# Kernel tuning notes

Hardware: AMD Instinct MI355X
Metric: run time of the kernel (lower is better)

## Reference

```python
import jax, jax.numpy as jnp
import numpy as np

HEADS = 8
DIM_HEAD = 64
DIM_COOR = 3
SCALE = (DIM_COOR * DIM_HEAD) ** -0.5


def setup_inputs() -> dict:
    key = jax.random.key(0)
    k1, k2, k3 = jax.random.split(key, 3)
    x = jax.random.normal(k1, (2, 2048, 256, 3), dtype=jnp.float32)
    w_qkv = jax.random.normal(k2, (1536, 256), dtype=jnp.float32)
    w_out = jax.random.normal(k3, (256, 512), dtype=jnp.float32)
    return {"x": x, "w_qkv": w_qkv, "w_out": w_out}


def reference(x, w_qkv, w_out):
    b, n, _, c = x.shape
    # VNLinear: contract feature dim, keep coord dim  -> [b, n, 3*h*d, c]
    qkv = jnp.einsum('bnic,oi->bnoc', x, w_qkv)
    q, k, v = jnp.split(qkv, 3, axis=-2)  # each [b, n, h*d, c]

    def to_heads(t):
        return t.reshape(b, n, HEADS, DIM_HEAD, c).transpose(0, 2, 1, 3, 4)  # b h n d c

    q, k, v = map(to_heads, (q, k, v))
    q = q * SCALE
    # scores sum over head-dim AND coordinate-dim
    sim = jnp.einsum('bhidc,bhjdc->bhij', q, k)
    attn = jax.nn.softmax(sim, axis=-1)
    out = jnp.einsum('bhij,bhjdc->bhidc', attn, v)  # coord dim preserved
    out = out.transpose(0, 2, 1, 3, 4).reshape(b, n, HEADS * DIM_HEAD, c)
    return jnp.einsum('bnic,oi->bnoc', out, w_out)
```

## Files before the change

### kernel.cpp

```cpp
#include <hip/hip_runtime.h>
#include <hip/hip_bf16.h>

#define SCALE 0.07216878364870322f

typedef __bf16 bf16x8 __attribute__((ext_vector_type(8)));
typedef float f32x16 __attribute__((ext_vector_type(16)));
typedef float f32x4v __attribute__((ext_vector_type(4)));
typedef unsigned int u32x4 __attribute__((ext_vector_type(4)));
typedef unsigned short u16;

#define MFMA(a, b, c) __builtin_amdgcn_mfma_f32_32x32x16_bf16(a, b, c, 0, 0, 0)

__device__ __forceinline__ u16 b16(float v) { return __builtin_bit_cast(u16, (__bf16)v); }
__device__ __forceinline__ float fb16(u16 u) {
    unsigned int t = (unsigned int)u << 16;
    return __builtin_bit_cast(float, t);
}
__device__ __forceinline__ unsigned int splitpack(float v) {
    u16 h = b16(v);
    float r = v - fb16(h);
    return (unsigned int)h | ((unsigned int)b16(r) << 16);
}
__device__ __forceinline__ unsigned int pack2(float a, float b) {
    return (unsigned int)b16(a) | ((unsigned int)b16(b) << 16);
}

__global__ __launch_bounds__(256) void qkv_mfma(const float* __restrict__ x,
                                                const float* __restrict__ wq,
                                                u16* __restrict__ Qhi, u16* __restrict__ Qlo,
                                                u16* __restrict__ Khi, u16* __restrict__ Klo,
                                                u16* __restrict__ Vf) {
    __shared__ unsigned int ldsr[2][32][196];
    const int tid = threadIdx.x;
    const int lane = tid & 63, w = tid >> 6, hf = lane >> 5, l31 = lane & 31;
    const int o0 = blockIdx.x * 64;
    const int n0 = blockIdx.y * 128;
    const int b = blockIdx.z;
    const int nw0 = n0 + w * 32;
    const int part = o0 >> 9;
    const int h = (o0 >> 6) & 7;
    const int bh = b * 8 + h;

    const float* xp = x + ((size_t)(b * 2048 + nw0 + l31)) * 768 + hf * 24;
    const float* wp0 = wq + (size_t)(o0 + l31) * 256 + hf * 8;
    const float* wp1 = wp0 + 32 * 256;

    f32x16 acc[3][2] = {};
    #pragma unroll 2
    for (int k0 = 0; k0 < 16; ++k0) {
        float xf[24], wf0[8], wf1[8];
        #pragma unroll
        for (int q = 0; q < 6; ++q) {
            f32x4v t = *(const f32x4v*)(xp + k0 * 48 + q * 4);
            xf[q * 4 + 0] = t[0]; xf[q * 4 + 1] = t[1];
            xf[q * 4 + 2] = t[2]; xf[q * 4 + 3] = t[3];
        }
        {
            f32x4v t0 = *(const f32x4v*)(wp0 + k0 * 16);
            f32x4v t1 = *(const f32x4v*)(wp0 + k0 * 16 + 4);
            f32x4v t2 = *(const f32x4v*)(wp1 + k0 * 16);
            f32x4v t3 = *(const f32x4v*)(wp1 + k0 * 16 + 4);
            #pragma unroll
            for (int e = 0; e < 4; ++e) {
                wf0[e] = t0[e]; wf0[4 + e] = t1[e];
                wf1[e] = t2[e]; wf1[4 + e] = t3[e];
            }
        }
        bf16x8 xh[3], xl[3], wh[2], wl[2];
        #pragma unroll
        for (int c = 0; c < 3; ++c)
            #pragma unroll
            for (int e = 0; e < 8; ++e) {
                float v = xf[e * 3 + c];
                __bf16 hi = (__bf16)v;
                xh[c][e] = hi;
                xl[c][e] = (__bf16)(v - (float)hi);
            }
        #pragma unroll
        for (int e = 0; e < 8; ++e) {
            { float v = wf0[e]; __bf16 hi = (__bf16)v; wh[0][e] = hi; wl[0][e] = (__bf16)(v - (float)hi); }
            { float v = wf1[e]; __bf16 hi = (__bf16)v; wh[1][e] = hi; wl[1][e] = (__bf16)(v - (float)hi); }
        }
        #pragma unroll
        for (int c = 0; c < 3; ++c)
            #pragma unroll
            for (int ot = 0; ot < 2; ++ot) {
                acc[c][ot] = MFMA(xh[c], wh[ot], acc[c][ot]);
                acc[c][ot] = MFMA(xl[c], wh[ot], acc[c][ot]);
                acc[c][ot] = MFMA(xh[c], wl[ot], acc[c][ot]);
            }
    }

    #pragma unroll
    for (int round = 0; round < 2; ++round) {
        __syncthreads();
        if ((w >> 1) == round) {
            unsigned int (*L)[196] = ldsr[w & 1];
            #pragma unroll
            for (int c = 0; c < 3; ++c)
                #pragma unroll
                for (int ot = 0; ot < 2; ++ot)
                    #pragma unroll
                    for (int r = 0; r < 16; ++r) {
                        float v = acc[c][ot][r];
                        if (part == 0) v *= SCALE;
                        int nn = (r & 3) + 8 * (r >> 2) + 4 * hf;
                        int dcol = 3 * (ot * 32 + l31) + c;
                        L[nn][dcol] = (part == 2) ? (unsigned int)b16(v) : splitpack(v);
                    }
            if (part < 2) {
                const int itqw = blockIdx.y * 4 + w;
                u16* bhp = (part == 0 ? Qhi : Khi) + (size_t)bh * 393216 + itqw * 6144 + lane * 8;
                u16* blp = (part == 0 ? Qlo : Klo) + (size_t)bh * 393216 + itqw * 6144 + lane * 8;
                #pragma unroll
                for (int ks = 0; ks < 12; ++ks) {
                    const unsigned int* p = &L[l31][ks * 16 + hf * 8];
                    u32x4 a = *(const u32x4*)p;
                    u32x4 bq = *(const u32x4*)(p + 4);
                    u32x4 hi = { (a[0] & 0xffffu) | (a[1] << 16), (a[2] & 0xffffu) | (a[3] << 16),
                                 (bq[0] & 0xffffu) | (bq[1] << 16), (bq[2] & 0xffffu) | (bq[3] << 16) };
                    u32x4 lo = { (a[0] >> 16) | (a[1] & 0xffff0000u), (a[2] >> 16) | (a[3] & 0xffff0000u),
                                 (bq[0] >> 16) | (bq[1] & 0xffff0000u), (bq[2] >> 16) | (bq[3] & 0xffff0000u) };
                    *(u32x4*)(bhp + ks * 512) = hi;
                    *(u32x4*)(blp + ks * 512) = lo;
                }
            } else {
                const int jt = nw0 >> 6;
                u16* vp = Vf + (size_t)bh * 393216 + jt * 12288 + lane * 8;
                #pragma unroll
                for (int jkk = 0; jkk < 2; ++jkk) {
                    const int jk = ((nw0 >> 4) + jkk) & 3;
                    #pragma unroll
                    for (int dcf = 0; dcf < 6; ++dcf) {
                        unsigned int t[8];
                        #pragma unroll
                        for (int e = 0; e < 8; ++e)
                            t[e] = L[jkk * 16 + hf * 8 + e][dcf * 32 + l31];
                        u32x4 pk = { (t[0] & 0xffffu) | (t[1] << 16), (t[2] & 0xffffu) | (t[3] << 16),
                                     (t[4] & 0xffffu) | (t[5] << 16), (t[6] & 0xffffu) | (t[7] << 16) };
                        *(u32x4*)(vp + (jk * 6 + dcf) * 512) = pk;
                    }
                }
            }
        }
    }
}

__global__ __launch_bounds__(256, 1) void attn_mfma(
    const u16* __restrict__ Qhi, const u16* __restrict__ Qlo,
    const u16* __restrict__ Khi, const u16* __restrict__ Klo,
    const u16* __restrict__ Vf, unsigned int* __restrict__ att2) {
    __shared__ __align__(16) u16 lds[36864];
    const int tid = threadIdx.x;
    const int lane = tid & 63;
    const int w = tid >> 6;
    const int hf = lane >> 5;
    const int bh = blockIdx.y;
    const int itq = blockIdx.x * 4 + w;

    bf16x8 qh[12], ql[12];
    {
        size_t qb = (((size_t)bh * 64 + itq) * 12 * 64 + lane) * 8;
        #pragma unroll
        for (int ks = 0; ks < 12; ++ks) {
            qh[ks] = *(const bf16x8*)(Qhi + qb + ks * 512);
            ql[ks] = *(const bf16x8*)(Qlo + qb + ks * 512);
        }
    }

    const char* gK = (const char*)Khi + (size_t)bh * 786432;
    const char* gL = (const char*)Klo + (size_t)bh * 786432;
    const char* gV = (const char*)Vf + (size_t)bh * 786432;
    const int soff = w * 6144 + lane * 16;

    u32x4 tr[18];
    #pragma unroll
    for (int cc = 0; cc < 6; ++cc) {
        tr[cc]      = *(const u32x4*)(gK + soff + cc * 1024);
        tr[6 + cc]  = *(const u32x4*)(gL + soff + cc * 1024);
        tr[12 + cc] = *(const u32x4*)(gV + soff + cc * 1024);
    }
    {
        char* lp = (char*)lds + soff;
        #pragma unroll
        for (int cc = 0; cc < 6; ++cc) {
            *(u32x4*)(lp + cc * 1024)         = tr[cc];
            *(u32x4*)(lp + 24576 + cc * 1024) = tr[6 + cc];
            *(u32x4*)(lp + 49152 + cc * 1024) = tr[12 + cc];
        }
    }
    __syncthreads();

    f32x16 o[6] = {};
    float m_run = -1e30f, l_run = 0.f;

    for (int jt = 0; jt < 32; ++jt) {
        f32x16 s00 = {}, s01 = {}, s10 = {}, s11 = {};
        #pragma unroll
        for (int mm = 0; mm < 6; ++mm) {
            const int k0 = mm * 2, k1 = mm * 2 + 1;
            bf16x8 kh00 = *(const bf16x8*)&lds[(size_t)((k0) * 64 + lane) * 8];
            bf16x8 kh01 = *(const bf16x8*)&lds[(size_t)((k1) * 64 + lane) * 8];
            bf16x8 kh10 = *(const bf16x8*)&lds[(size_t)((12 + k0) * 64 + lane) * 8];
            bf16x8 kh11 = *(const bf16x8*)&lds[(size_t)((12 + k1) * 64 + lane) * 8];
            bf16x8 kl00 = *(const bf16x8*)&lds[12288 + (size_t)((k0) * 64 + lane) * 8];
            bf16x8 kl01 = *(const bf16x8*)&lds[12288 + (size_t)((k1) * 64 + lane) * 8];
            bf16x8 kl10 = *(const bf16x8*)&lds[12288 + (size_t)((12 + k0) * 64 + lane) * 8];
            bf16x8 kl11 = *(const bf16x8*)&lds[12288 + (size_t)((12 + k1) * 64 + lane) * 8];
            s00 = MFMA(kh00, qh[k0], s00);
            s10 = MFMA(kh10, qh[k0], s10);
            s01 = MFMA(kh01, qh[k1], s01);
            s11 = MFMA(kh11, qh[k1], s11);
            s00 = MFMA(kh00, ql[k0], s00);
            s10 = MFMA(kh10, ql[k0], s10);
            s01 = MFMA(kh01, ql[k1], s01);
            s11 = MFMA(kh11, ql[k1], s11);
            s00 = MFMA(kl00, qh[k0], s00);
            s10 = MFMA(kl10, qh[k0], s10);
            s01 = MFMA(kl01, qh[k1], s01);
            s11 = MFMA(kl11, qh[k1], s11);
        }

        if (jt + 1 < 32) {
            const size_t joff = (size_t)(jt + 1) * 24576 + soff;
            #pragma unroll
            for (int cc = 0; cc < 6; ++cc) {
                tr[cc]      = *(const u32x4*)(gK + joff + cc * 1024);
                tr[6 + cc]  = *(const u32x4*)(gL + joff + cc * 1024);
                tr[12 + cc] = *(const u32x4*)(gV + joff + cc * 1024);
            }
        }

        f32x16 sj0 = s00 + s01;
        f32x16 sj1 = s10 + s11;
        float rm = m_run;
        #pragma unroll
        for (int r = 0; r < 16; ++r) rm = fmaxf(rm, fmaxf(sj0[r], sj1[r]));
        rm = fmaxf(rm, __shfl_xor(rm, 32, 64));
        float sc = __expf(m_run - rm);
        float rs = 0.f;
        #pragma unroll
        for (int r = 0; r < 16; ++r) {
            sj0[r] = __expf(sj0[r] - rm); rs += sj0[r];
            sj1[r] = __expf(sj1[r] - rm); rs += sj1[r];
        }
        rs += __shfl_xor(rs, 32, 64);
        l_run = l_run * sc + rs;
        m_run = rm;
        #pragma unroll
        for (int d = 0; d < 6; ++d) o[d] = o[d] * sc;

        bf16x8 pf[4];
        {
            unsigned int pk[8], X[8];
            #pragma unroll
            for (int g = 0; g < 8; ++g) {
                pk[g] = pack2(sj0[2 * g], sj0[2 * g + 1]);
                X[g] = (unsigned int)__shfl_xor((int)pk[g], 32, 64);
            }
            u32x4 f0 = {hf ? X[2] : pk[0], hf ? X[3] : pk[1], hf ? pk[2] : X[0], hf ? pk[3] : X[1]};
            u32x4 f1 = {hf ? X[6] : pk[4], hf ? X[7] : pk[5], hf ? pk[6] : X[4], hf ? pk[7] : X[5]};
            pf[0] = __builtin_bit_cast(bf16x8, f0);
            pf[1] = __builtin_bit_cast(bf16x8, f1);
            #pragma unroll
            for (int g = 0; g < 8; ++g) {
                pk[g] = pack2(sj1[2 * g], sj1[2 * g + 1]);
                X[g] = (unsigned int)__shfl_xor((int)pk[g], 32, 64);
            }
            u32x4 f2 = {hf ? X[2] : pk[0], hf ? X[3] : pk[1], hf ? pk[2] : X[0], hf ? pk[3] : X[1]};
            u32x4 f3 = {hf ? X[6] : pk[4], hf ? X[7] : pk[5], hf ? pk[6] : X[4], hf ? pk[7] : X[5]};
            pf[2] = __builtin_bit_cast(bf16x8, f2);
            pf[3] = __builtin_bit_cast(bf16x8, f3);
        }

        #pragma unroll
        for (int jk = 0; jk < 4; ++jk)
            #pragma unroll
            for (int d = 0; d < 6; ++d) {
                bf16x8 vf = *(const bf16x8*)&lds[24576 + (size_t)((jk * 6 + d) * 64 + lane) * 8];
                o[d] = MFMA(vf, pf[jk], o[d]);
            }

        if (jt + 1 < 32) {
            __syncthreads();
            char* lp = (char*)lds + soff;
            #pragma unroll
            for (int cc = 0; cc < 6; ++cc) {
                *(u32x4*)(lp + cc * 1024)         = tr[cc];
                *(u32x4*)(lp + 24576 + cc * 1024) = tr[6 + cc];
                *(u32x4*)(lp + 49152 + cc * 1024) = tr[12 + cc];
            }
            __syncthreads();
        }
    }

    float inv = 1.0f / l_run;
    const int b2 = bh >> 3, hh = bh & 7;
    const int i31 = lane & 31;
    #pragma unroll
    for (int d = 0; d < 6; ++d)
        #pragma unroll
        for (int r = 0; r < 16; ++r) {
            int dc = d * 32 + (r & 3) + 8 * (r >> 2) + 4 * hf;
            int dd = dc / 3, cc = dc - dd * 3;
            int hd = hh * 64 + dd;
            int ks = hd >> 4, e = hd & 7;
            int ln = i31 | (((hd >> 3) & 1) << 5);
            size_t off = ((((size_t)(b2 * 3 + cc) * 32 + ks) * 64 + itq) * 512 + (size_t)ln * 8 + e);
            float v = o[d][r] * inv;
            att2[off] = splitpack(v);
        }
}

__global__ __launch_bounds__(256) void out_mfma(const unsigned int* __restrict__ att2,
                                                const float* __restrict__ wo,
                                                float* __restrict__ out) {
    const int tid = threadIdx.x, lane = tid & 63, w = tid >> 6, hf = lane >> 5, l31 = lane & 31;
    const int o0 = blockIdx.x * 32;
    const int n5 = blockIdx.y * 4 + w;
    const int b = blockIdx.z;
    const float* wp = wo + (size_t)(o0 + l31) * 512 + hf * 8;
    const unsigned int* ap = att2 + ((size_t)(b * 3) * 2048 + n5) * 512 + (size_t)lane * 8;
    f32x16 acc[3] = {};
    #pragma unroll 2
    for (int ks = 0; ks < 32; ++ks) {
        bf16x8 wh, wl;
        {
            f32x4v t0 = *(const f32x4v*)(wp + ks * 16);
            f32x4v t1 = *(const f32x4v*)(wp + ks * 16 + 4);
            #pragma unroll
            for (int e = 0; e < 4; ++e) {
                { float v = t0[e]; __bf16 hi = (__bf16)v; wh[e] = hi; wl[e] = (__bf16)(v - (float)hi); }
                { float v = t1[e]; __bf16 hi = (__bf16)v; wh[4 + e] = hi; wl[4 + e] = (__bf16)(v - (float)hi); }
            }
        }
        #pragma unroll
        for (int c = 0; c < 3; ++c) {
            const unsigned int* pc = ap + (size_t)c * 1048576 + ks * 32768;
            u32x4 a0 = *(const u32x4*)pc;
            u32x4 a1 = *(const u32x4*)(pc + 4);
            union { bf16x8 v; u32x4 u; } H, Lo;
            H.u  = { (a0[0] & 0xffffu) | (a0[1] << 16), (a0[2] & 0xffffu) | (a0[3] << 16),
                     (a1[0] & 0xffffu) | (a1[1] << 16), (a1[2] & 0xffffu) | (a1[3] << 16) };
            Lo.u = { (a0[0] >> 16) | (a0[1] & 0xffff0000u), (a0[2] >> 16) | (a0[3] & 0xffff0000u),
                     (a1[0] >> 16) | (a1[1] & 0xffff0000u), (a1[2] >> 16) | (a1[3] & 0xffff0000u) };
            acc[c] = MFMA(H.v, wh, acc[c]);
            acc[c] = MFMA(Lo.v, wh, acc[c]);
            acc[c] = MFMA(H.v, wl, acc[c]);
        }
    }
    #pragma unroll
    for (int r = 0; r < 16; ++r) {
        int n = (n5 << 5) + (r & 3) + 8 * (r >> 2) + 4 * hf;
        size_t off = ((size_t)(b * 2048 + n) * 256 + o0 + l31) * 3;
        out[off]     = acc[0][r];
        out[off + 1] = acc[1][r];
        out[off + 2] = acc[2][r];
    }
}

extern "C" void kernel_launch(void* const* d_in, const int* in_sizes, int n_in,
                              void* d_out, int out_size, void* d_ws, size_t ws_size,
                              hipStream_t stream) {
    const float* x     = (const float*)d_in[0];
    const float* w_qkv = (const float*)d_in[1];
    const float* w_out = (const float*)d_in[2];
    float* out = (float*)d_out;

    const size_t NB = (size_t)16 * 2048 * 192;
    u16* Qhi = (u16*)d_ws;
    u16* Qlo = Qhi + NB;
    u16* Khi = Qlo + NB;
    u16* Klo = Khi + NB;
    u16* Vf  = Klo + NB;
    unsigned int* att2 = (unsigned int*)(Vf + NB);

    qkv_mfma<<<dim3(24, 16, 2), 256, 0, stream>>>(x, w_qkv, Qhi, Qlo, Khi, Klo, Vf);
    attn_mfma<<<dim3(16, 16), 256, 0, stream>>>(Qhi, Qlo, Khi, Klo, Vf, att2);
    out_mfma<<<dim3(8, 16, 2), 256, 0, stream>>>(att2, w_out, out);
}
```

Before: 251.8 us.

## Split attention KV sequence across two wave groups and merge softmax partials

The attention block doubles to 512 threads. Two groups of four waves each process half of the key/value tiles for the same query rows, using separate LDS buffers, and their partial (m, l, O) states are merged through LDS at the end. The softmax moves to exp2 by folding log2(e) into the Q scale, and it adds a lazy rescale that skips updating O and l unless the running max grows by more than 8. This doubles the number of active waves and halves each wave's serial KV loop to raise MFMA utilisation. The cost is twice the LDS per block, an extra reduction phase, and larger intermediate exponents from the lazy-max threshold.

After: 371.3 us. 1.47x slower.

```diff
diff --git a/kernel.cpp b/kernel.cpp
--- a/kernel.cpp
+++ b/kernel.cpp
@@ -2,6 +2,7 @@
 #include <hip/hip_bf16.h>
 
 #define SCALE 0.07216878364870322f
+#define LOG2E 1.4426950408889634f
 
 typedef __bf16 bf16x8 __attribute__((ext_vector_type(8)));
 typedef float f32x16 __attribute__((ext_vector_type(16)));
@@ -103,7 +104,7 @@
                     #pragma unroll
                     for (int r = 0; r < 16; ++r) {
                         float v = acc[c][ot][r];
-                        if (part == 0) v *= SCALE;
+                        if (part == 0) v *= (SCALE * LOG2E);
                         int nn = (r & 3) + 8 * (r >> 2) + 4 * hf;
                         int dcol = 3 * (ot * 32 + l31) + c;
                         L[nn][dcol] = (part == 2) ? (unsigned int)b16(v) : splitpack(v);
@@ -146,17 +147,19 @@
     }
 }
 
-__global__ __launch_bounds__(256, 1) void attn_mfma(
+__global__ __launch_bounds__(512, 2) void attn_mfma(
     const u16* __restrict__ Qhi, const u16* __restrict__ Qlo,
     const u16* __restrict__ Khi, const u16* __restrict__ Klo,
     const u16* __restrict__ Vf, unsigned int* __restrict__ att2) {
-    __shared__ __align__(16) u16 lds[36864];
+    __shared__ __align__(16) u16 lds[2][36864];
     const int tid = threadIdx.x;
     const int lane = tid & 63;
     const int w = tid >> 6;
+    const int half = w >> 2;
+    const int wl = w & 3;
     const int hf = lane >> 5;
     const int bh = blockIdx.y;
-    const int itq = blockIdx.x * 4 + w;
+    const int itq = blockIdx.x * 4 + wl;
 
     bf16x8 qh[12], ql[12];
     {
@@ -168,10 +171,11 @@
         }
     }
 
-    const char* gK = (const char*)Khi + (size_t)bh * 786432;
-    const char* gL = (const char*)Klo + (size_t)bh * 786432;
-    const char* gV = (const char*)Vf + (size_t)bh * 786432;
-    const int soff = w * 6144 + lane * 16;
+    const char* gK = (const char*)Khi + (size_t)bh * 786432 + (size_t)half * 393216;
+    const char* gL = (const char*)Klo + (size_t)bh * 786432 + (size_t)half * 393216;
+    const char* gV = (const char*)Vf  + (size_t)bh * 786432 + (size_t)half * 393216;
+    const int soff = wl * 6144 + lane * 16;
+    u16* ldsH = lds[half];
 
     u32x4 tr[18];
     #pragma unroll
@@ -181,7 +185,7 @@
         tr[12 + cc] = *(const u32x4*)(gV + soff + cc * 1024);
     }
     {
-        char* lp = (char*)lds + soff;
+        char* lp = (char*)ldsH + soff;
         #pragma unroll
         for (int cc = 0; cc < 6; ++cc) {
             *(u32x4*)(lp + cc * 1024)         = tr[cc];
@@ -194,19 +198,19 @@
     f32x16 o[6] = {};
     float m_run = -1e30f, l_run = 0.f;
 
-    for (int jt = 0; jt < 32; ++jt) {
+    for (int jt = 0; jt < 16; ++jt) {
         f32x16 s00 = {}, s01 = {}, s10 = {}, s11 = {};
         #pragma unroll
         for (int mm = 0; mm < 6; ++mm) {
             const int k0 = mm * 2, k1 = mm * 2 + 1;
-            bf16x8 kh00 = *(const bf16x8*)&lds[(size_t)((k0) * 64 + lane) * 8];
-            bf16x8 kh01 = *(const bf16x8*)&lds[(size_t)((k1) * 64 + lane) * 8];
-            bf16x8 kh10 = *(const bf16x8*)&lds[(size_t)((12 + k0) * 64 + lane) * 8];
-            bf16x8 kh11 = *(const bf16x8*)&lds[(size_t)((12 + k1) * 64 + lane) * 8];
-            bf16x8 kl00 = *(const bf16x8*)&lds[12288 + (size_t)((k0) * 64 + lane) * 8];
-            bf16x8 kl01 = *(const bf16x8*)&lds[12288 + (size_t)((k1) * 64 + lane) * 8];
-            bf16x8 kl10 = *(const bf16x8*)&lds[12288 + (size_t)((12 + k0) * 64 + lane) * 8];
-            bf16x8 kl11 = *(const bf16x8*)&lds[12288 + (size_t)((12 + k1) * 64 + lane) * 8];
+            bf16x8 kh00 = *(const bf16x8*)&ldsH[(size_t)((k0) * 64 + lane) * 8];
+            bf16x8 kh01 = *(const bf16x8*)&ldsH[(size_t)((k1) * 64 + lane) * 8];
+            bf16x8 kh10 = *(const bf16x8*)&ldsH[(size_t)((12 + k0) * 64 + lane) * 8];
+            bf16x8 kh11 = *(const bf16x8*)&ldsH[(size_t)((12 + k1) * 64 + lane) * 8];
+            bf16x8 kl00 = *(const bf16x8*)&ldsH[12288 + (size_t)((k0) * 64 + lane) * 8];
+            bf16x8 kl01 = *(const bf16x8*)&ldsH[12288 + (size_t)((k1) * 64 + lane) * 8];
+            bf16x8 kl10 = *(const bf16x8*)&ldsH[12288 + (size_t)((12 + k0) * 64 + lane) * 8];
+            bf16x8 kl11 = *(const bf16x8*)&ldsH[12288 + (size_t)((12 + k1) * 64 + lane) * 8];
             s00 = MFMA(kh00, qh[k0], s00);
             s10 = MFMA(kh10, qh[k0], s10);
             s01 = MFMA(kh01, qh[k1], s01);
@@ -221,7 +225,7 @@
             s11 = MFMA(kl11, qh[k1], s11);
         }
 
-        if (jt + 1 < 32) {
+        if (jt + 1 < 16) {
             const size_t joff = (size_t)(jt + 1) * 24576 + soff;
             #pragma unroll
             for (int cc = 0; cc < 6; ++cc) {
@@ -233,22 +237,26 @@
 
         f32x16 sj0 = s00 + s01;
         f32x16 sj1 = s10 + s11;
-        float rm = m_run;
-        #pragma unroll
-        for (int r = 0; r < 16; ++r) rm = fmaxf(rm, fmaxf(sj0[r], sj1[r]));
-        rm = fmaxf(rm, __shfl_xor(rm, 32, 64));
-        float sc = __expf(m_run - rm);
+        float pm = -1e30f;
+        #pragma unroll
+        for (int r = 0; r < 16; ++r) pm = fmaxf(pm, fmaxf(sj0[r], sj1[r]));
+        pm = fmaxf(pm, __shfl_xor(pm, 32, 64));
+        if (!__all(pm <= m_run + 8.0f)) {
+            float mnew = fmaxf(m_run, pm);
+            float sc = exp2f(m_run - mnew);
+            l_run *= sc;
+            #pragma unroll
+            for (int d = 0; d < 6; ++d) o[d] = o[d] * sc;
+            m_run = mnew;
+        }
         float rs = 0.f;
         #pragma unroll
         for (int r = 0; r < 16; ++r) {
-            sj0[r] = __expf(sj0[r] - rm); rs += sj0[r];
-            sj1[r] = __expf(sj1[r] - rm); rs += sj1[r];
+            sj0[r] = exp2f(sj0[r] - m_run); rs += sj0[r];
+            sj1[r] = exp2f(sj1[r] - m_run); rs += sj1[r];
         }
         rs += __shfl_xor(rs, 32, 64);
-        l_run = l_run * sc + rs;
-        m_run = rm;
-        #pragma unroll
-        for (int d = 0; d < 6; ++d) o[d] = o[d] * sc;
+        l_run += rs;
 
         bf16x8 pf[4];
         {
@@ -277,13 +285,13 @@
         for (int jk = 0; jk < 4; ++jk)
             #pragma unroll
             for (int d = 0; d < 6; ++d) {
-                bf16x8 vf = *(const bf16x8*)&lds[24576 + (size_t)((jk * 6 + d) * 64 + lane) * 8];
+                bf16x8 vf = *(const bf16x8*)&ldsH[24576 + (size_t)((jk * 6 + d) * 64 + lane) * 8];
                 o[d] = MFMA(vf, pf[jk], o[d]);
             }
 
-        if (jt + 1 < 32) {
+        if (jt + 1 < 16) {
             __syncthreads();
-            char* lp = (char*)lds + soff;
+            char* lp = (char*)ldsH + soff;
             #pragma unroll
             for (int cc = 0; cc < 6; ++cc) {
                 *(u32x4*)(lp + cc * 1024)         = tr[cc];
@@ -294,22 +302,48 @@
         }
     }
 
-    float inv = 1.0f / l_run;
-    const int b2 = bh >> 3, hh = bh & 7;
-    const int i31 = lane & 31;
-    #pragma unroll
-    for (int d = 0; d < 6; ++d)
-        #pragma unroll
-        for (int r = 0; r < 16; ++r) {
-            int dc = d * 32 + (r & 3) + 8 * (r >> 2) + 4 * hf;
-            int dd = dc / 3, cc = dc - dd * 3;
-            int hd = hh * 64 + dd;
-            int ks = hd >> 4, e = hd & 7;
-            int ln = i31 | (((hd >> 3) & 1) << 5);
-            size_t off = ((((size_t)(b2 * 3 + cc) * 32 + ks) * 64 + itq) * 512 + (size_t)ln * 8 + e);
-            float v = o[d][r] * inv;
-            att2[off] = splitpack(v);
-        }
+    float* LM = (float*)&lds[0][0];
+    __syncthreads();
+    if (half == 1) {
+        #pragma unroll
+        for (int d = 0; d < 6; ++d)
+            #pragma unroll
+            for (int q = 0; q < 4; ++q) {
+                f32x4v t = { o[d][4 * q], o[d][4 * q + 1], o[d][4 * q + 2], o[d][4 * q + 3] };
+                *(f32x4v*)&LM[(((wl * 24 + d * 4 + q) * 64) + lane) * 4] = t;
+            }
+        LM[24576 + (wl * 64 + lane) * 2]     = m_run;
+        LM[24576 + (wl * 64 + lane) * 2 + 1] = l_run;
+    }
+    __syncthreads();
+    if (half == 0) {
+        float mb = LM[24576 + (wl * 64 + lane) * 2];
+        float lb = LM[24576 + (wl * 64 + lane) * 2 + 1];
+        float mm = fmaxf(m_run, mb);
+        float wa = exp2f(m_run - mm);
+        float wb = exp2f(mb - mm);
+        float inv = 1.0f / (l_run * wa + lb * wb);
+        const int b2 = bh >> 3, hh = bh & 7;
+        const int i31 = lane & 31;
+        #pragma unroll
+        for (int d = 0; d < 6; ++d)
+            #pragma unroll
+            for (int q = 0; q < 4; ++q) {
+                f32x4v t = *(const f32x4v*)&LM[(((wl * 24 + d * 4 + q) * 64) + lane) * 4];
+                #pragma unroll
+                for (int j = 0; j < 4; ++j) {
+                    int r = 4 * q + j;
+                    float v = (o[d][r] * wa + t[j] * wb) * inv;
+                    int dc = d * 32 + (r & 3) + 8 * (r >> 2) + 4 * hf;
+                    int dd = dc / 3, cc = dc - dd * 3;
+                    int hd = hh * 64 + dd;
+                    int ks = hd >> 4, e = hd & 7;
+                    int ln = i31 | (((hd >> 3) & 1) << 5);
+                    size_t off = ((((size_t)(b2 * 3 + cc) * 32 + ks) * 64 + itq) * 512 + (size_t)ln * 8 + e);
+                    att2[off] = splitpack(v);
+                }
+            }
+    }
 }
 
 __global__ __launch_bounds__(256) void out_mfma(const unsigned int* __restrict__ att2,
@@ -376,6 +410,6 @@
     unsigned int* att2 = (unsigned int*)(Vf + NB);
 
     qkv_mfma<<<dim3(24, 16, 2), 256, 0, stream>>>(x, w_qkv, Qhi, Qlo, Khi, Klo, Vf);
-    attn_mfma<<<dim3(16, 16), 256, 0, stream>>>(Qhi, Qlo, Khi, Klo, Vf, att2);
+    attn_mfma<<<dim3(16, 16), 512, 0, stream>>>(Qhi, Qlo, Khi, Klo, Vf, att2);
     out_mfma<<<dim3(8, 16, 2), 256, 0, stream>>>(att2, w_out, out);
 }
```

## Split attention over key halves with combine kernel and lazy rescaling

Applied to the files above, without the earlier changes.

Splits the key/value sequence into two halves processed by separate blocks (split-K flash attention), writing partial bf16 outputs plus running max/sum, and adds a combine kernel that merges them and writes the att2 layout. This doubles the attention grid from 256 blocks to 512 so more CUs are busy, and raises launch bounds to allow two blocks per CU. It also folds log2(e) into the Q scale so exp2f can be used, and skips rescaling of the output accumulator unless the running max grows by more than 8. The costs are an extra kernel launch, extra global traffic for the partials, and bf16 rounding of the partial outputs, which may lose precision.

New measurement: 292.7 us. 1.16x slower.

```diff
diff --git a/kernel.cpp b/kernel.cpp
--- a/kernel.cpp
+++ b/kernel.cpp
@@ -2,6 +2,7 @@
 #include <hip/hip_bf16.h>
 
 #define SCALE 0.07216878364870322f
+#define LOG2E 1.4426950408889634f
 
 typedef __bf16 bf16x8 __attribute__((ext_vector_type(8)));
 typedef float f32x16 __attribute__((ext_vector_type(16)));
@@ -103,7 +104,7 @@
                     #pragma unroll
                     for (int r = 0; r < 16; ++r) {
                         float v = acc[c][ot][r];
-                        if (part == 0) v *= SCALE;
+                        if (part == 0) v *= (SCALE * LOG2E);
                         int nn = (r & 3) + 8 * (r >> 2) + 4 * hf;
                         int dcol = 3 * (ot * 32 + l31) + c;
                         L[nn][dcol] = (part == 2) ? (unsigned int)b16(v) : splitpack(v);
@@ -146,16 +147,17 @@
     }
 }
 
-__global__ __launch_bounds__(256, 1) void attn_mfma(
+__global__ __launch_bounds__(256, 2) void attn_mfma(
     const u16* __restrict__ Qhi, const u16* __restrict__ Qlo,
     const u16* __restrict__ Khi, const u16* __restrict__ Klo,
-    const u16* __restrict__ Vf, unsigned int* __restrict__ att2) {
+    const u16* __restrict__ Vf, u16* __restrict__ Opart, float* __restrict__ MLp) {
     __shared__ __align__(16) u16 lds[36864];
     const int tid = threadIdx.x;
     const int lane = tid & 63;
     const int w = tid >> 6;
     const int hf = lane >> 5;
     const int bh = blockIdx.y;
+    const int half = blockIdx.z;
     const int itq = blockIdx.x * 4 + w;
 
     bf16x8 qh[12], ql[12];
@@ -168,9 +170,9 @@
         }
     }
 
-    const char* gK = (const char*)Khi + (size_t)bh * 786432;
-    const char* gL = (const char*)Klo + (size_t)bh * 786432;
-    const char* gV = (const char*)Vf + (size_t)bh * 786432;
+    const char* gK = (const char*)Khi + (size_t)bh * 786432 + (size_t)half * 393216;
+    const char* gL = (const char*)Klo + (size_t)bh * 786432 + (size_t)half * 393216;
+    const char* gV = (const char*)Vf  + (size_t)bh * 786432 + (size_t)half * 393216;
     const int soff = w * 6144 + lane * 16;
 
     u32x4 tr[18];
@@ -194,7 +196,7 @@
     f32x16 o[6] = {};
     float m_run = -1e30f, l_run = 0.f;
 
-    for (int jt = 0; jt < 32; ++jt) {
+    for (int jt = 0; jt < 16; ++jt) {
         f32x16 s00 = {}, s01 = {}, s10 = {}, s11 = {};
         #pragma unroll
         for (int mm = 0; mm < 6; ++mm) {
@@ -221,7 +223,7 @@
             s11 = MFMA(kl11, qh[k1], s11);
         }
 
-        if (jt + 1 < 32) {
+        if (jt + 1 < 16) {
             const size_t joff = (size_t)(jt + 1) * 24576 + soff;
             #pragma unroll
             for (int cc = 0; cc < 6; ++cc) {
@@ -233,22 +235,26 @@
 
         f32x16 sj0 = s00 + s01;
         f32x16 sj1 = s10 + s11;
-        float rm = m_run;
-        #pragma unroll
-        for (int r = 0; r < 16; ++r) rm = fmaxf(rm, fmaxf(sj0[r], sj1[r]));
-        rm = fmaxf(rm, __shfl_xor(rm, 32, 64));
-        float sc = __expf(m_run - rm);
+        float pm = -1e30f;
+        #pragma unroll
+        for (int r = 0; r < 16; ++r) pm = fmaxf(pm, fmaxf(sj0[r], sj1[r]));
+        pm = fmaxf(pm, __shfl_xor(pm, 32, 64));
+        if (!__all(pm <= m_run + 8.0f)) {
+            float mnew = fmaxf(m_run, pm);
+            float sc = exp2f(m_run - mnew);
+            l_run *= sc;
+            #pragma unroll
+            for (int d = 0; d < 6; ++d) o[d] = o[d] * sc;
+            m_run = mnew;
+        }
         float rs = 0.f;
         #pragma unroll
         for (int r = 0; r < 16; ++r) {
-            sj0[r] = __expf(sj0[r] - rm); rs += sj0[r];
-            sj1[r] = __expf(sj1[r] - rm); rs += sj1[r];
+            sj0[r] = exp2f(sj0[r] - m_run); rs += sj0[r];
+            sj1[r] = exp2f(sj1[r] - m_run); rs += sj1[r];
         }
         rs += __shfl_xor(rs, 32, 64);
-        l_run = l_run * sc + rs;
-        m_run = rm;
-        #pragma unroll
-        for (int d = 0; d < 6; ++d) o[d] = o[d] * sc;
+        l_run += rs;
 
         bf16x8 pf[4];
         {
@@ -281,7 +287,7 @@
                 o[d] = MFMA(vf, pf[jk], o[d]);
             }
 
-        if (jt + 1 < 32) {
+        if (jt + 1 < 16) {
             __syncthreads();
             char* lp = (char*)lds + soff;
             #pragma unroll
@@ -294,20 +300,48 @@
         }
     }
 
-    float inv = 1.0f / l_run;
+    const int tI = bh * 64 + itq;
+    u16* Op = Opart + ((size_t)(half * 1024 + tI) * 96) * 64 + lane;
+    #pragma unroll
+    for (int d = 0; d < 6; ++d)
+        #pragma unroll
+        for (int r = 0; r < 16; ++r)
+            Op[(d * 16 + r) * 64] = b16(o[d][r]);
+    float* mlp = MLp + (size_t)(half * 1024 + tI) * 128 + lane * 2;
+    mlp[0] = m_run;
+    mlp[1] = l_run;
+}
+
+__global__ __launch_bounds__(256) void attn_combine(const u16* __restrict__ Opart,
+                                                    const float* __restrict__ MLp,
+                                                    unsigned int* __restrict__ att2) {
+    const int tid = threadIdx.x, lane = tid & 63, w = tid >> 6, hf = lane >> 5;
+    const int tI = blockIdx.x * 4 + w;
+    const int bh = tI >> 6, itq = tI & 63;
+    const float* mla = MLp + (size_t)tI * 128 + lane * 2;
+    const float* mlb = MLp + (size_t)(1024 + tI) * 128 + lane * 2;
+    float ma = mla[0], la = mla[1];
+    float mb = mlb[0], lb = mlb[1];
+    float mm = fmaxf(ma, mb);
+    float wa = exp2f(ma - mm), wb = exp2f(mb - mm);
+    float inv = 1.0f / (la * wa + lb * wb);
+    const u16* Oa = Opart + ((size_t)tI * 96) * 64 + lane;
+    const u16* Ob = Opart + ((size_t)(1024 + tI) * 96) * 64 + lane;
     const int b2 = bh >> 3, hh = bh & 7;
     const int i31 = lane & 31;
     #pragma unroll
     for (int d = 0; d < 6; ++d)
         #pragma unroll
         for (int r = 0; r < 16; ++r) {
+            float va = fb16(Oa[(d * 16 + r) * 64]);
+            float vb = fb16(Ob[(d * 16 + r) * 64]);
+            float v = (va * wa + vb * wb) * inv;
             int dc = d * 32 + (r & 3) + 8 * (r >> 2) + 4 * hf;
             int dd = dc / 3, cc = dc - dd * 3;
             int hd = hh * 64 + dd;
             int ks = hd >> 4, e = hd & 7;
             int ln = i31 | (((hd >> 3) & 1) << 5);
             size_t off = ((((size_t)(b2 * 3 + cc) * 32 + ks) * 64 + itq) * 512 + (size_t)ln * 8 + e);
-            float v = o[d][r] * inv;
             att2[off] = splitpack(v);
         }
 }
@@ -373,9 +407,12 @@
     u16* Khi = Qlo + NB;
     u16* Klo = Khi + NB;
     u16* Vf  = Klo + NB;
-    unsigned int* att2 = (unsigned int*)(Vf + NB);
+    u16* Opart = Vf + NB;
+    float* MLp = (float*)(Opart + 2 * NB);
+    unsigned int* att2 = (unsigned int*)Qhi;
 
     qkv_mfma<<<dim3(24, 16, 2), 256, 0, stream>>>(x, w_qkv, Qhi, Qlo, Khi, Klo, Vf);
-    attn_mfma<<<dim3(16, 16), 256, 0, stream>>>(Qhi, Qlo, Khi, Klo, Vf, att2);
+    attn_mfma<<<dim3(16, 16, 2), 256, 0, stream>>>(Qhi, Qlo, Khi, Klo, Vf, Opart, MLp);
+    attn_combine<<<dim3(256), 256, 0, stream>>>(Opart, MLp, att2);
     out_mfma<<<dim3(8, 16, 2), 256, 0, stream>>>(att2, w_out, out);
 }
```

## Restructure attention with 16x16 MFMA, double-buffered async LDS loads, lazy rescale

Applied to the files above, without the earlier changes.

The attention kernel is rewritten to use 16x16x32 MFMA tiles with 8 waves per block, each handling 16 query rows, and the QKV kernel writes Q, K and V in matching layouts. K and V tiles are staged into a double-buffered LDS area with global_load_lds, so one barrier per tile replaces the register round-trip and two barriers. Softmax moves to exp2 by folding log2(e) into the Q scale, and the running-max rescale is skipped while the new max stays within a threshold. The costs are more shuffles to rebuild the P operand, a larger LDS footprint, and a block-index remap of heads across the grid.

Measured after the change: 225.6 us. -10.4%, faster.

```diff
diff --git a/kernel.cpp b/kernel.cpp
--- a/kernel.cpp
+++ b/kernel.cpp
@@ -2,6 +2,7 @@
 #include <hip/hip_bf16.h>
 
 #define SCALE 0.07216878364870322f
+#define LOG2E 1.4426950408889634f
 
 typedef __bf16 bf16x8 __attribute__((ext_vector_type(8)));
 typedef float f32x16 __attribute__((ext_vector_type(16)));
@@ -10,6 +11,7 @@
 typedef unsigned short u16;
 
 #define MFMA(a, b, c) __builtin_amdgcn_mfma_f32_32x32x16_bf16(a, b, c, 0, 0, 0)
+#define MFMA16(a, b, c) __builtin_amdgcn_mfma_f32_16x16x32_bf16(a, b, c, 0, 0, 0)
 
 __device__ __forceinline__ u16 b16(float v) { return __builtin_bit_cast(u16, (__bf16)v); }
 __device__ __forceinline__ float fb16(u16 u) {
@@ -23,6 +25,10 @@
 }
 __device__ __forceinline__ unsigned int pack2(float a, float b) {
     return (unsigned int)b16(a) | ((unsigned int)b16(b) << 16);
+}
+__device__ __forceinline__ void gload16(const void* g, void* l) {
+    __builtin_amdgcn_global_load_lds((const __attribute__((address_space(1))) void*)g,
+                                     (__attribute__((address_space(3))) void*)l, 16, 0, 0);
 }
 
 __global__ __launch_bounds__(256) void qkv_mfma(const float* __restrict__ x,
@@ -33,6 +39,7 @@
     __shared__ unsigned int ldsr[2][32][196];
     const int tid = threadIdx.x;
     const int lane = tid & 63, w = tid >> 6, hf = lane >> 5, l31 = lane & 31;
+    const int lq = lane & 15, gq = lane >> 4;
     const int o0 = blockIdx.x * 64;
     const int n0 = blockIdx.y * 128;
     const int b = blockIdx.z;
@@ -103,212 +110,189 @@
                     #pragma unroll
                     for (int r = 0; r < 16; ++r) {
                         float v = acc[c][ot][r];
-                        if (part == 0) v *= SCALE;
+                        if (part == 0) v *= (SCALE * LOG2E);
                         int nn = (r & 3) + 8 * (r >> 2) + 4 * hf;
                         int dcol = 3 * (ot * 32 + l31) + c;
                         L[nn][dcol] = (part == 2) ? (unsigned int)b16(v) : splitpack(v);
                     }
             if (part < 2) {
-                const int itqw = blockIdx.y * 4 + w;
-                u16* bhp = (part == 0 ? Qhi : Khi) + (size_t)bh * 393216 + itqw * 6144 + lane * 8;
-                u16* blp = (part == 0 ? Qlo : Klo) + (size_t)bh * 393216 + itqw * 6144 + lane * 8;
+                const int jt = nw0 >> 6;
+                u16* baseH = (part == 0 ? Qhi : Khi);
+                u16* baseL = (part == 0 ? Qlo : Klo);
                 #pragma unroll
-                for (int ks = 0; ks < 12; ++ks) {
-                    const unsigned int* p = &L[l31][ks * 16 + hf * 8];
-                    u32x4 a = *(const u32x4*)p;
-                    u32x4 bq = *(const u32x4*)(p + 4);
-                    u32x4 hi = { (a[0] & 0xffffu) | (a[1] << 16), (a[2] & 0xffffu) | (a[3] << 16),
-                                 (bq[0] & 0xffffu) | (bq[1] << 16), (bq[2] & 0xffffu) | (bq[3] << 16) };
-                    u32x4 lo = { (a[0] >> 16) | (a[1] & 0xffff0000u), (a[2] >> 16) | (a[3] & 0xffff0000u),
-                                 (bq[0] >> 16) | (bq[1] & 0xffff0000u), (bq[2] >> 16) | (bq[3] & 0xffff0000u) };
-                    *(u32x4*)(bhp + ks * 512) = hi;
-                    *(u32x4*)(blp + ks * 512) = lo;
+                for (int is = 0; is < 2; ++is)
+                    #pragma unroll
+                    for (int kc = 0; kc < 6; ++kc) {
+                        const unsigned int* p = &L[is * 16 + lq][kc * 32 + gq * 8];
+                        u32x4 a = *(const u32x4*)p;
+                        u32x4 bq = *(const u32x4*)(p + 4);
+                        u32x4 hi = { (a[0] & 0xffffu) | (a[1] << 16), (a[2] & 0xffffu) | (a[3] << 16),
+                                     (bq[0] & 0xffffu) | (bq[1] << 16), (bq[2] & 0xffffu) | (bq[3] << 16) };
+                        u32x4 lo = { (a[0] >> 16) | (a[1] & 0xffff0000u), (a[2] >> 16) | (a[3] & 0xffff0000u),
+                                     (bq[0] >> 16) | (bq[1] & 0xffff0000u), (bq[2] >> 16) | (bq[3] & 0xffff0000u) };
+                        size_t off;
+                        if (part == 0)
+                            off = ((size_t)(bh * 128 + (nw0 >> 4) + is) * 6 + kc) * 512 + lane * 8;
+                        else
+                            off = ((size_t)(bh * 32 + jt) * 24 + ((((nw0 >> 4) & 3) + is) * 6 + kc)) * 512 + lane * 8;
+                        *(u32x4*)(baseH + off) = hi;
+                        *(u32x4*)(baseL + off) = lo;
+                    }
+            } else {
+                const int jt = nw0 >> 6, jc = (nw0 >> 5) & 1;
+                u16* vp = Vf + ((size_t)(bh * 32 + jt) * 24 + jc) * 512 + lane * 8;
+                #pragma unroll
+                for (int d = 0; d < 12; ++d) {
+                    unsigned int t[8];
+                    #pragma unroll
+                    for (int e = 0; e < 8; ++e)
+                        t[e] = L[gq * 8 + e][d * 16 + lq];
+                    u32x4 pk = { (t[0] & 0xffffu) | (t[1] << 16), (t[2] & 0xffffu) | (t[3] << 16),
+                                 (t[4] & 0xffffu) | (t[5] << 16), (t[6] & 0xffffu) | (t[7] << 16) };
+                    *(u32x4*)(vp + d * 1024) = pk;
                 }
-            } else {
-                const int jt = nw0 >> 6;
-                u16* vp = Vf + (size_t)bh * 393216 + jt * 12288 + lane * 8;
-                #pragma unroll
-                for (int jkk = 0; jkk < 2; ++jkk) {
-                    const int jk = ((nw0 >> 4) + jkk) & 3;
-                    #pragma unroll
-                    for (int dcf = 0; dcf < 6; ++dcf) {
-                        unsigned int t[8];
-                        #pragma unroll
-                        for (int e = 0; e < 8; ++e)
-                            t[e] = L[jkk * 16 + hf * 8 + e][dcf * 32 + l31];
-                        u32x4 pk = { (t[0] & 0xffffu) | (t[1] << 16), (t[2] & 0xffffu) | (t[3] << 16),
-                                     (t[4] & 0xffffu) | (t[5] << 16), (t[6] & 0xffffu) | (t[7] << 16) };
-                        *(u32x4*)(vp + (jk * 6 + dcf) * 512) = pk;
-                    }
-                }
-            }
-        }
-    }
-}
-
-__global__ __launch_bounds__(256, 1) void attn_mfma(
+            }
+        }
+    }
+}
+
+__global__ __launch_bounds__(512) void attn_mfma(
     const u16* __restrict__ Qhi, const u16* __restrict__ Qlo,
     const u16* __restrict__ Khi, const u16* __restrict__ Klo,
     const u16* __restrict__ Vf, unsigned int* __restrict__ att2) {
-    __shared__ __align__(16) u16 lds[36864];
+    __shared__ __align__(16) u16 lds[2][36864];
     const int tid = threadIdx.x;
     const int lane = tid & 63;
     const int w = tid >> 6;
-    const int hf = lane >> 5;
-    const int bh = blockIdx.y;
-    const int itq = blockIdx.x * 4 + w;
-
-    bf16x8 qh[12], ql[12];
+    const int g = lane >> 4;
+    const int i = lane & 15;
+    const int id = blockIdx.x;
+    const int bh = (id & 7) * 2 + (id >> 7);
+    const int itile = (id >> 3) & 15;
+    const int i0 = itile * 128 + w * 16;
+
+    bf16x8 qh[6], ql[6];
     {
-        size_t qb = (((size_t)bh * 64 + itq) * 12 * 64 + lane) * 8;
-        #pragma unroll
-        for (int ks = 0; ks < 12; ++ks) {
-            qh[ks] = *(const bf16x8*)(Qhi + qb + ks * 512);
-            ql[ks] = *(const bf16x8*)(Qlo + qb + ks * 512);
+        size_t qb = ((size_t)(bh * 128 + (i0 >> 4)) * 6) * 512 + (size_t)lane * 8;
+        #pragma unroll
+        for (int kc = 0; kc < 6; ++kc) {
+            qh[kc] = *(const bf16x8*)(Qhi + qb + kc * 512);
+            ql[kc] = *(const bf16x8*)(Qlo + qb + kc * 512);
         }
     }
 
     const char* gK = (const char*)Khi + (size_t)bh * 786432;
     const char* gL = (const char*)Klo + (size_t)bh * 786432;
     const char* gV = (const char*)Vf + (size_t)bh * 786432;
-    const int soff = w * 6144 + lane * 16;
-
-    u32x4 tr[18];
-    #pragma unroll
-    for (int cc = 0; cc < 6; ++cc) {
-        tr[cc]      = *(const u32x4*)(gK + soff + cc * 1024);
-        tr[6 + cc]  = *(const u32x4*)(gL + soff + cc * 1024);
-        tr[12 + cc] = *(const u32x4*)(gV + soff + cc * 1024);
-    }
-    {
-        char* lp = (char*)lds + soff;
-        #pragma unroll
-        for (int cc = 0; cc < 6; ++cc) {
-            *(u32x4*)(lp + cc * 1024)         = tr[cc];
-            *(u32x4*)(lp + 24576 + cc * 1024) = tr[6 + cc];
-            *(u32x4*)(lp + 49152 + cc * 1024) = tr[12 + cc];
-        }
-    }
+    const int t16 = tid * 16;
+
+    auto stage = [&](int buf, int jt) {
+        const size_t jo = (size_t)jt * 24576 + t16;
+        char* dst = (char*)&lds[buf][0] + t16;
+        #pragma unroll
+        for (int s = 0; s < 3; ++s) {
+            gload16(gK + jo + s * 8192, dst + s * 8192);
+            gload16(gL + jo + s * 8192, dst + 24576 + s * 8192);
+            gload16(gV + jo + s * 8192, dst + 49152 + s * 8192);
+        }
+    };
+
+    stage(0, 0);
     __syncthreads();
-
-    f32x16 o[6] = {};
+    int cur = 0;
+
+    f32x4v o[12] = {};
     float m_run = -1e30f, l_run = 0.f;
+    const int sl0 = ((g & 1) << 5) + i;
+    const int sl1 = sl0 + 16;
+    const bool ghi = (g >> 1) != 0;
 
     for (int jt = 0; jt < 32; ++jt) {
-        f32x16 s00 = {}, s01 = {}, s10 = {}, s11 = {};
-        #pragma unroll
-        for (int mm = 0; mm < 6; ++mm) {
-            const int k0 = mm * 2, k1 = mm * 2 + 1;
-            bf16x8 kh00 = *(const bf16x8*)&lds[(size_t)((k0) * 64 + lane) * 8];
-            bf16x8 kh01 = *(const bf16x8*)&lds[(size_t)((k1) * 64 + lane) * 8];
-            bf16x8 kh10 = *(const bf16x8*)&lds[(size_t)((12 + k0) * 64 + lane) * 8];
-            bf16x8 kh11 = *(const bf16x8*)&lds[(size_t)((12 + k1) * 64 + lane) * 8];
-            bf16x8 kl00 = *(const bf16x8*)&lds[12288 + (size_t)((k0) * 64 + lane) * 8];
-            bf16x8 kl01 = *(const bf16x8*)&lds[12288 + (size_t)((k1) * 64 + lane) * 8];
-            bf16x8 kl10 = *(const bf16x8*)&lds[12288 + (size_t)((12 + k0) * 64 + lane) * 8];
-            bf16x8 kl11 = *(const bf16x8*)&lds[12288 + (size_t)((12 + k1) * 64 + lane) * 8];
-            s00 = MFMA(kh00, qh[k0], s00);
-            s10 = MFMA(kh10, qh[k0], s10);
-            s01 = MFMA(kh01, qh[k1], s01);
-            s11 = MFMA(kh11, qh[k1], s11);
-            s00 = MFMA(kh00, ql[k0], s00);
-            s10 = MFMA(kh10, ql[k0], s10);
-            s01 = MFMA(kh01, ql[k1], s01);
-            s11 = MFMA(kh11, ql[k1], s11);
-            s00 = MFMA(kl00, qh[k0], s00);
-            s10 = MFMA(kl10, qh[k0], s10);
-            s01 = MFMA(kl01, qh[k1], s01);
-            s11 = MFMA(kl11, qh[k1], s11);
-        }
-
-        if (jt + 1 < 32) {
-            const size_t joff = (size_t)(jt + 1) * 24576 + soff;
-            #pragma unroll
-            for (int cc = 0; cc < 6; ++cc) {
-                tr[cc]      = *(const u32x4*)(gK + joff + cc * 1024);
-                tr[6 + cc]  = *(const u32x4*)(gL + joff + cc * 1024);
-                tr[12 + cc] = *(const u32x4*)(gV + joff + cc * 1024);
-            }
-        }
-
-        f32x16 sj0 = s00 + s01;
-        f32x16 sj1 = s10 + s11;
-        float rm = m_run;
-        #pragma unroll
-        for (int r = 0; r < 16; ++r) rm = fmaxf(rm, fmaxf(sj0[r], sj1[r]));
-        rm = fmaxf(rm, __shfl_xor(rm, 32, 64));
-        float sc = __expf(m_run - rm);
+        if (jt + 1 < 32) stage(cur ^ 1, jt + 1);
+        const u16* L = &lds[cur][0];
+
+        f32x4v s4[4] = {};
+        #pragma unroll
+        for (int kc = 0; kc < 6; ++kc) {
+            bf16x8 kh[4], kl[4];
+            #pragma unroll
+            for (int js = 0; js < 4; ++js) {
+                kh[js] = *(const bf16x8*)&L[(unsigned)((js * 6 + kc) * 512) + lane * 8];
+                kl[js] = *(const bf16x8*)&L[12288u + (unsigned)((js * 6 + kc) * 512) + lane * 8];
+            }
+            #pragma unroll
+            for (int js = 0; js < 4; ++js) s4[js] = MFMA16(kh[js], qh[kc], s4[js]);
+            #pragma unroll
+            for (int js = 0; js < 4; ++js) s4[js] = MFMA16(kh[js], ql[kc], s4[js]);
+            #pragma unroll
+            for (int js = 0; js < 4; ++js) s4[js] = MFMA16(kl[js], qh[kc], s4[js]);
+        }
+
+        float pm = -1e30f;
+        #pragma unroll
+        for (int js = 0; js < 4; ++js)
+            #pragma unroll
+            for (int r = 0; r < 4; ++r) pm = fmaxf(pm, s4[js][r]);
+        pm = fmaxf(pm, __shfl_xor(pm, 16, 64));
+        pm = fmaxf(pm, __shfl_xor(pm, 32, 64));
+        if (!__all(pm <= m_run + 8.0f)) {
+            float mnew = fmaxf(m_run, pm);
+            float sc = exp2f(m_run - mnew);
+            l_run *= sc;
+            #pragma unroll
+            for (int d = 0; d < 12; ++d) o[d] = o[d] * sc;
+            m_run = mnew;
+        }
         float rs = 0.f;
-        #pragma unroll
-        for (int r = 0; r < 16; ++r) {
-            sj0[r] = __expf(sj0[r] - rm); rs += sj0[r];
-            sj1[r] = __expf(sj1[r] - rm); rs += sj1[r];
-        }
+        unsigned int w0[4], w1[4];
+        #pragma unroll
+        for (int js = 0; js < 4; ++js) {
+            float p0 = exp2f(s4[js][0] - m_run), p1 = exp2f(s4[js][1] - m_run);
+            float p2 = exp2f(s4[js][2] - m_run), p3 = exp2f(s4[js][3] - m_run);
+            rs += (p0 + p1) + (p2 + p3);
+            w0[js] = pack2(p0, p1);
+            w1[js] = pack2(p2, p3);
+        }
+        rs += __shfl_xor(rs, 16, 64);
         rs += __shfl_xor(rs, 32, 64);
-        l_run = l_run * sc + rs;
-        m_run = rm;
-        #pragma unroll
-        for (int d = 0; d < 6; ++d) o[d] = o[d] * sc;
-
-        bf16x8 pf[4];
-        {
-            unsigned int pk[8], X[8];
-            #pragma unroll
-            for (int g = 0; g < 8; ++g) {
-                pk[g] = pack2(sj0[2 * g], sj0[2 * g + 1]);
-                X[g] = (unsigned int)__shfl_xor((int)pk[g], 32, 64);
-            }
-            u32x4 f0 = {hf ? X[2] : pk[0], hf ? X[3] : pk[1], hf ? pk[2] : X[0], hf ? pk[3] : X[1]};
-            u32x4 f1 = {hf ? X[6] : pk[4], hf ? X[7] : pk[5], hf ? pk[6] : X[4], hf ? pk[7] : X[5]};
-            pf[0] = __builtin_bit_cast(bf16x8, f0);
-            pf[1] = __builtin_bit_cast(bf16x8, f1);
-            #pragma unroll
-            for (int g = 0; g < 8; ++g) {
-                pk[g] = pack2(sj1[2 * g], sj1[2 * g + 1]);
-                X[g] = (unsigned int)__shfl_xor((int)pk[g], 32, 64);
-            }
-            u32x4 f2 = {hf ? X[2] : pk[0], hf ? X[3] : pk[1], hf ? pk[2] : X[0], hf ? pk[3] : X[1]};
-            u32x4 f3 = {hf ? X[6] : pk[4], hf ? X[7] : pk[5], hf ? pk[6] : X[4], hf ? pk[7] : X[5]};
-            pf[2] = __builtin_bit_cast(bf16x8, f2);
-            pf[3] = __builtin_bit_cast(bf16x8, f3);
-        }
-
-        #pragma unroll
-        for (int jk = 0; jk < 4; ++jk)
-            #pragma unroll
-            for (int d = 0; d < 6; ++d) {
-                bf16x8 vf = *(const bf16x8*)&lds[24576 + (size_t)((jk * 6 + d) * 64 + lane) * 8];
-                o[d] = MFMA(vf, pf[jk], o[d]);
-            }
+        l_run += rs;
+
+        #pragma unroll
+        for (int c = 0; c < 2; ++c) {
+            u32x4 F;
+            { unsigned a0 = __shfl((int)w0[2 * c], sl0, 64), a1 = __shfl((int)w0[2 * c + 1], sl0, 64); F[0] = ghi ? a1 : a0; }
+            { unsigned a0 = __shfl((int)w1[2 * c], sl0, 64), a1 = __shfl((int)w1[2 * c + 1], sl0, 64); F[1] = ghi ? a1 : a0; }
+            { unsigned a0 = __shfl((int)w0[2 * c], sl1, 64), a1 = __shfl((int)w0[2 * c + 1], sl1, 64); F[2] = ghi ? a1 : a0; }
+            { unsigned a0 = __shfl((int)w1[2 * c], sl1, 64), a1 = __shfl((int)w1[2 * c + 1], sl1, 64); F[3] = ghi ? a1 : a0; }
+            bf16x8 pb = __builtin_bit_cast(bf16x8, F);
+            #pragma unroll
+            for (int d = 0; d < 12; ++d) {
+                bf16x8 vf = *(const bf16x8*)&L[24576u + (unsigned)((d * 2 + c) * 512) + lane * 8];
+                o[d] = MFMA16(vf, pb, o[d]);
+            }
+        }
 
         if (jt + 1 < 32) {
             __syncthreads();
-            char* lp = (char*)lds + soff;
-            #pragma unroll
-            for (int cc = 0; cc < 6; ++cc) {
-                *(u32x4*)(lp + cc * 1024)         = tr[cc];
-                *(u32x4*)(lp + 24576 + cc * 1024) = tr[6 + cc];
-                *(u32x4*)(lp + 49152 + cc * 1024) = tr[12 + cc];
-            }
-            __syncthreads();
+            cur ^= 1;
         }
     }
 
     float inv = 1.0f / l_run;
     const int b2 = bh >> 3, hh = bh & 7;
-    const int i31 = lane & 31;
+    const int ig = i0 + i;
+    const int itq = ig >> 5, i31 = ig & 31;
     #pragma unroll
-    for (int d = 0; d < 6; ++d)
-        #pragma unroll
-        for (int r = 0; r < 16; ++r) {
-            int dc = d * 32 + (r & 3) + 8 * (r >> 2) + 4 * hf;
-            int dd = dc / 3, cc = dc - dd * 3;
+    for (int d = 0; d < 12; ++d)
+        #pragma unroll
+        for (int r = 0; r < 4; ++r) {
+            int dc = d * 16 + g * 4 + r;
+            int dd = dc / 3, cc2 = dc - dd * 3;
             int hd = hh * 64 + dd;
             int ks = hd >> 4, e = hd & 7;
             int ln = i31 | (((hd >> 3) & 1) << 5);
-            size_t off = ((((size_t)(b2 * 3 + cc) * 32 + ks) * 64 + itq) * 512 + (size_t)ln * 8 + e);
-            float v = o[d][r] * inv;
-            att2[off] = splitpack(v);
+            size_t off = (((size_t)(b2 * 3 + cc2) * 32 + ks) * 64 + itq) * 512 + (size_t)ln * 8 + e;
+            att2[off] = splitpack(o[d][r] * inv);
         }
 }
 
@@ -376,6 +360,6 @@
     unsigned int* att2 = (unsigned int*)(Vf + NB);
 
     qkv_mfma<<<dim3(24, 16, 2), 256, 0, stream>>>(x, w_qkv, Qhi, Qlo, Khi, Klo, Vf);
-    attn_mfma<<<dim3(16, 16), 256, 0, stream>>>(Qhi, Qlo, Khi, Klo, Vf, att2);
+    attn_mfma<<<dim3(256), 512, 0, stream>>>(Qhi, Qlo, Khi, Klo, Vf, att2);
     out_mfma<<<dim3(8, 16, 2), 256, 0, stream>>>(att2, w_out, out);
 }
```
